# Performance work log

Measured on AMD Instinct MI355X. Metric: run time of the kernel, lower is better.

## Reference

```python
import jax, jax.numpy as jnp
import numpy as np

N_HEADS = 8
D_K = 256
SCALE = D_K ** -0.5


def setup_inputs() -> dict:
    key = jax.random.key(0)
    k1, k2, k3 = jax.random.split(key, 3)
    B, C, H, W = 8, 256, 32, 32
    x = jax.random.normal(k1, (B, C, H, W), dtype=jnp.float32)
    Wp = jax.random.normal(k2, (C, N_HEADS * D_K * 3), dtype=jnp.float32) * (C ** -0.5)
    bp = jnp.zeros((N_HEADS * D_K * 3,), dtype=jnp.float32)
    Wo = jax.random.normal(k3, (N_HEADS * D_K, C), dtype=jnp.float32) * ((N_HEADS * D_K) ** -0.5)
    bo = jnp.zeros((C,), dtype=jnp.float32)
    return {"x": x, "Wp": Wp, "bp": bp, "Wo": Wo, "bo": bo}


def reference(x, Wp, bp, Wo, bo):
    B, C, H, W = x.shape
    S = H * W
    # [B,C,H,W] -> [B,S,C] tokens
    xt = x.reshape(B, C, S).transpose(0, 2, 1)
    qkv = (xt @ Wp + bp).reshape(B, S, N_HEADS, 3 * D_K)
    q, k, v = jnp.split(qkv, 3, axis=-1)  # each [B,S,H,dk]
    attn = jnp.einsum('bihd,bjhd->bijh', q, k) * SCALE
    attn = jax.nn.softmax(attn, axis=2)  # over j (keys)
    res = jnp.einsum('bijh,bjhd->bihd', attn, v).reshape(B, S, N_HEADS * D_K)
    res = res @ Wo + bo + xt  # residual
    return res.transpose(0, 2, 1).reshape(B, C, H, W)
```

## Files before the change

kernel.cpp:

```cpp
#include <hip/hip_runtime.h>

#define NH    8
#define DK    256
#define SS    1024
#define QSCALE 0.09016844136947155f
#define TSH   8192

using frag8  = __attribute__((ext_vector_type(8))) short;
using f32x4  = __attribute__((ext_vector_type(4))) float;
using f32x16 = __attribute__((ext_vector_type(16))) float;

__device__ __forceinline__ unsigned short f2bf(float f) {
    unsigned int u = __float_as_uint(f);
    return (unsigned short)((u + 0x7FFFu + ((u >> 16) & 1u)) >> 16);
}
__device__ __forceinline__ unsigned int pk2bf(float lo, float hi) {
    unsigned int ul = __float_as_uint(lo), uh = __float_as_uint(hi);
    ul += 0x7FFFu + ((ul >> 16) & 1u);
    uh += 0x7FFFu + ((uh >> 16) & 1u);
    return (ul >> 16) | (uh & 0xFFFF0000u);
}

__device__ __forceinline__ void load_lds16(const void* g, void* l) {
    __builtin_amdgcn_global_load_lds(
        (const __attribute__((address_space(1))) unsigned int*)g,
        (__attribute__((address_space(3))) unsigned int*)l, 16, 0, 0);
}


__global__ __launch_bounds__(256) void k0_all(
    const float* __restrict__ x,  unsigned short* __restrict__ xb,
    const float* __restrict__ Wp, unsigned short* __restrict__ Wpt,
    const float* __restrict__ Wo, unsigned short* __restrict__ Wot)
{
    __shared__ float tile[32][33];
    const int bid = blockIdx.x;
    const float* in; unsigned short* out; int R, C, c0, r0;
    if (bid < 2048) {
        int rr = bid;
        in = x + (size_t)(rr >> 8) * 256 * 1024;
        out = xb + (size_t)(rr >> 8) * 256 * 1024;
        R = 256; C = 1024; c0 = (rr & 31) * 32; r0 = ((rr >> 5) & 7) * 32;
    } else if (bid < 3584) {
        int rr = bid - 2048;
        in = Wp; out = Wpt; R = 256; C = 6144;
        c0 = (rr % 192) * 32; r0 = (rr / 192) * 32;
    } else {
        int rr = bid - 3584;
        in = Wo; out = Wot; R = 2048; C = 256;
        c0 = (rr & 7) * 32; r0 = (rr >> 3) * 32;
    }
    const int tx = threadIdx.x & 31, ty = threadIdx.x >> 5;
#pragma unroll
    for (int j = 0; j < 4; j++)
        tile[ty + j * 8][tx] = in[(size_t)(r0 + ty + j * 8) * C + c0 + tx];
    __syncthreads();
#pragma unroll
    for (int j = 0; j < 4; j++)
        out[(size_t)(c0 + ty + j * 8) * R + r0 + tx] = f2bf(tile[tx][ty + j * 8]);
}

__global__ __launch_bounds__(512) void k1_qkv(
    const unsigned short* __restrict__ xb, const unsigned short* __restrict__ Wpt,
    const float* __restrict__ bp,
    unsigned short* __restrict__ qb, unsigned short* __restrict__ kb,
    unsigned short* __restrict__ vb)
{
    __shared__ unsigned short As[2][256 * 32];
    __shared__ unsigned short Bs[2][128 * 32];
    const int t = threadIdx.x;
    const int wave = t >> 6, lane = t & 63;
    const int quad = lane >> 4, l16 = lane & 15;
    const int n0 = blockIdx.x * 128, m0 = blockIdx.y * 256;
    const int b = m0 >> 10, s0 = m0 & 1023;
    const int lr = lane >> 2, lc = (lane & 3) * 8;

    const int h = n0 / 768;
    const int rem = n0 - h * 768;
    const int tt = rem >> 8;

    const int aoff = (tt < 2) ? (wave & 1) * 64 : (wave >> 1) * 64;
    const int boff = (tt < 2) ? (wave >> 1) * 64 : (wave & 1) * 64;

    const unsigned short* Ag = xb + (size_t)(b * 1024 + s0) * 256;
    const unsigned short* Bg = Wpt + (size_t)n0 * 256;

    f32x4 acc[4][4];
#pragma unroll
    for (int i = 0; i < 4; i++)
#pragma unroll
        for (int j = 0; j < 4; j++) acc[i][j] = (f32x4){0.f, 0.f, 0.f, 0.f};

    auto stage = [&](int buf, int kt) {
        const int k0 = kt * 32;
#pragma unroll
        for (int j = 0; j < 2; j++) {
            int ch = wave + j * 8;
            load_lds16(Ag + (size_t)(ch * 16 + lr) * 256 + k0 + lc, &As[buf][ch * 512]);
        }
        load_lds16(Bg + (size_t)(wave * 16 + lr) * 256 + k0 + lc, &Bs[buf][wave * 512]);
    };

    stage(0, 0);
    __syncthreads();

    for (int kt = 0; kt < 8; kt++) {
        const int cur = kt & 1;
        if (kt < 7) stage(cur ^ 1, kt + 1);
        const unsigned short* Fa = (tt < 2) ? &Bs[cur][0] : &As[cur][0];
        const unsigned short* Fb = (tt < 2) ? &As[cur][0] : &Bs[cur][0];
        frag8 af[4], bf[4];
#pragma unroll
        for (int i = 0; i < 4; i++)
            af[i] = *(const frag8*)(&Fa[(aoff + i * 16 + l16) * 32 + quad * 8]);
#pragma unroll
        for (int j = 0; j < 4; j++)
            bf[j] = *(const frag8*)(&Fb[(boff + j * 16 + l16) * 32 + quad * 8]);
#pragma unroll
        for (int i = 0; i < 4; i++)
#pragma unroll
            for (int j = 0; j < 4; j++)
                acc[i][j] = __builtin_amdgcn_mfma_f32_16x16x32_bf16(af[i], bf[j], acc[i][j], 0, 0, 0);
        __syncthreads();
    }

    const int dcol0 = rem & 255;
    const size_t bh = (size_t)(b * NH + h);

    if (tt < 2) {
        const float sc = (tt == 0) ? QSCALE : 1.0f;
        unsigned short* dst = (tt == 0 ? qb : kb) + bh * 32 * TSH;
#pragma unroll
        for (int i = 0; i < 4; i++) {
            const int mloc = aoff + i * 16;
            float4 b4 = *(const float4*)(&bp[n0 + mloc + quad * 4]);
            const int octet = ((dcol0 + mloc) >> 3) + (quad >> 1);
            const int drem4 = (quad & 1) * 4;
#pragma unroll
            for (int j = 0; j < 4; j++) {
                const int s = s0 + boff + j * 16 + l16;
                unsigned short* cell = dst + (size_t)(s >> 5) * TSH
                                     + octet * 256 + (s & 31) * 8 + drem4;
                uint2 st;
                st.x = pk2bf((acc[i][j][0] + b4.x) * sc, (acc[i][j][1] + b4.y) * sc);
                st.y = pk2bf((acc[i][j][2] + b4.z) * sc, (acc[i][j][3] + b4.w) * sc);
                *(uint2*)cell = st;
            }
        }
    } else {
        unsigned short* dst = vb + bh * 32 * TSH;
        const int chunk = (quad & 1) * 2048;
        const int jjb = (quad & 2) * 2;
        float bias[4];
#pragma unroll
        for (int j = 0; j < 4; j++) bias[j] = bp[n0 + boff + j * 16 + l16];
#pragma unroll
        for (int j = 0; j < 4; j++) {
            int d = dcol0 + boff + j * 16 + l16;
#pragma unroll
            for (int i = 0; i < 4; i++) {
                int g = ((aoff >> 4) + i) & 1;
                size_t tile = (size_t)((s0 + aoff + i * 16) >> 5) * TSH;
                uint2 st;
                st.x = pk2bf(acc[i][j][0] + bias[j], acc[i][j][1] + bias[j]);
                st.y = pk2bf(acc[i][j][2] + bias[j], acc[i][j][3] + bias[j]);
                *(uint2*)(&dst[tile + g * 4096 + chunk + d * 8 + jjb]) = st;
            }
        }
    }
}

__global__ __launch_bounds__(256, 2) void k2_attn(
    const unsigned short* __restrict__ qb, const unsigned short* __restrict__ kb,
    const unsigned short* __restrict__ vb, unsigned short* __restrict__ ob)
{
    __shared__ unsigned short Ks[2][TSH];
    __shared__ unsigned short Vs[2][TSH];

    const int t = threadIdx.x;
    const int wave = t >> 6, lane = t & 63;
    const int l32 = lane & 31, hw = lane >> 5;

    const int flat = blockIdx.x;
    const int xcd = flat & 7, tt2 = flat >> 3;
    const int qt = tt2 & 7;
    const int bh = xcd * 8 + (tt2 >> 3);

    const int qrow0 = qt * 128 + wave * 32;

    frag8 qf[16];
    {
        const unsigned short* qp = qb + ((size_t)bh * 32 + qt * 4 + wave) * TSH
                                 + hw * 256 + l32 * 8;
#pragma unroll
        for (int s = 0; s < 16; s++) qf[s] = *(const frag8*)(qp + s * 512);
    }

    f32x16 acc[8];
#pragma unroll
    for (int nb = 0; nb < 8; nb++)
#pragma unroll
        for (int r = 0; r < 16; r++) acc[nb][r] = 0.f;
    float lsum = 0.f;

    const unsigned short* kstg = kb + (size_t)bh * 32 * TSH + wave * 2048 + lane * 8;
    const unsigned short* vstg = vb + (size_t)bh * 32 * TSH + wave * 2048 + lane * 8;

    auto prefetch = [&](int buf, int kt) {
#pragma unroll
        for (int j = 0; j < 4; j++) {
            load_lds16(kstg + (size_t)kt * TSH + j * 512, &Ks[buf][wave * 2048 + j * 512]);
            load_lds16(vstg + (size_t)kt * TSH + j * 512, &Vs[buf][wave * 2048 + j * 512]);
        }
    };

    auto body = [&](const unsigned short* Kb, const unsigned short* Vb) {
        f32x16 sa0, sa1;
#pragma unroll
        for (int r = 0; r < 16; r++) { sa0[r] = 0.f; sa1[r] = 0.f; }
        __builtin_amdgcn_s_setprio(1);
#pragma unroll
        for (int s = 0; s < 16; s += 2) {
            frag8 kf0 = *(const frag8*)(Kb + (2 * s + hw) * 256 + l32 * 8);
            frag8 kf1 = *(const frag8*)(Kb + (2 * s + 2 + hw) * 256 + l32 * 8);
            sa0 = __builtin_amdgcn_mfma_f32_32x32x16_bf16(kf0, qf[s], sa0, 0, 0, 0);
            sa1 = __builtin_amdgcn_mfma_f32_32x32x16_bf16(kf1, qf[s + 1], sa1, 0, 0, 0);
        }
        __builtin_amdgcn_s_setprio(0);
        float p[16];
#pragma unroll
        for (int e = 0; e < 16; e++) {
            p[e] = exp2f(sa0[e] + sa1[e]);
            lsum += p[e];
        }
        frag8 pf[2];
#pragma unroll
        for (int g = 0; g < 2; g++) {
            uint4 w;
            w.x = pk2bf(p[g * 8 + 0], p[g * 8 + 1]);
            w.y = pk2bf(p[g * 8 + 2], p[g * 8 + 3]);
            w.z = pk2bf(p[g * 8 + 4], p[g * 8 + 5]);
            w.w = pk2bf(p[g * 8 + 6], p[g * 8 + 7]);
            pf[g] = *(frag8*)&w;
        }
        __builtin_amdgcn_s_setprio(1);
#pragma unroll
        for (int g = 0; g < 2; g++)
#pragma unroll
            for (int nb = 0; nb < 8; nb++) {
                frag8 vf = *(const frag8*)(Vb + (g * 2 + hw) * 2048 + (nb * 32 + l32) * 8);
                acc[nb] = __builtin_amdgcn_mfma_f32_32x32x16_bf16(pf[g], vf, acc[nb], 0, 0, 0);
            }
        __builtin_amdgcn_s_setprio(0);
    };

    prefetch(0, 0);
    asm volatile("s_waitcnt vmcnt(0)" ::: "memory");
    __builtin_amdgcn_s_barrier();
    for (int kt = 0; kt < 30; kt += 2) {
        prefetch(1, kt + 1);
        asm volatile("s_waitcnt vmcnt(8)" ::: "memory");
        __builtin_amdgcn_s_barrier();
        body(&Ks[0][0], &Vs[0][0]);
        __builtin_amdgcn_s_barrier();
        prefetch(0, kt + 2);
        asm volatile("s_waitcnt vmcnt(8)" ::: "memory");
        __builtin_amdgcn_s_barrier();
        body(&Ks[1][0], &Vs[1][0]);
        __builtin_amdgcn_s_barrier();
    }
    prefetch(1, 31);
    asm volatile("s_waitcnt vmcnt(8)" ::: "memory");
    __builtin_amdgcn_s_barrier();
    body(&Ks[0][0], &Vs[0][0]);
    asm volatile("s_waitcnt vmcnt(0)" ::: "memory");
    __builtin_amdgcn_s_barrier();
    body(&Ks[1][0], &Vs[1][0]);

    lsum += __shfl_xor(lsum, 32);
    const float linv = 1.f / lsum;

    unsigned short* og = ob + ((size_t)bh * SS + qrow0) * DK + l32;
#pragma unroll
    for (int r = 0; r < 16; r++) {
        const int rowl = (r & 3) + 8 * (r >> 2) + 4 * hw;
        const float li = __shfl(linv, rowl, 64);
        unsigned short* orow = og + (size_t)rowl * DK;
#pragma unroll
        for (int nb = 0; nb < 8; nb++)
            orow[nb * 32] = f2bf(acc[nb][r] * li);
    }
}

__global__ __launch_bounds__(256) void k3_proj(
    const unsigned short* __restrict__ ob, const unsigned short* __restrict__ Wot,
    const float* __restrict__ bo, const float* __restrict__ x,
    float* __restrict__ out)
{
    __shared__ unsigned short As[2][2][2048];
    __shared__ unsigned short Bs[2][2][2048];
    const int t = threadIdx.x;
    const int wave = t >> 6, lane = t & 63;
    const int quad = lane >> 4, l16 = lane & 15;
    const int n0 = blockIdx.x * 64, m0 = blockIdx.y * 64;
    const int b = m0 >> 10, s0 = m0 & 1023;
    const int mq = (wave >> 1) * 32, nq = (wave & 1) * 32;
    const int lr = lane >> 2, lc = (lane & 3) * 8;

    const unsigned short* Bg = Wot + (size_t)n0 * 2048;

    f32x4 acc[2][2];
#pragma unroll
    for (int i = 0; i < 2; i++)
#pragma unroll
        for (int j = 0; j < 2; j++) acc[i][j] = (f32x4){0.f, 0.f, 0.f, 0.f};

    auto stage = [&](int buf, int kt) {
        const int k0 = kt * 64;
        const int h = k0 >> 8, d0 = k0 & 255;
        const unsigned short* Ag = ob + (size_t)((b * 8 + h) * 1024 + s0) * 256 + d0;
#pragma unroll
        for (int sl = 0; sl < 2; sl++) {
            load_lds16(Ag + (size_t)(wave * 16 + lr) * 256 + sl * 32 + lc, &As[buf][sl][wave * 512]);
            load_lds16(Bg + (size_t)(wave * 16 + lr) * 2048 + k0 + sl * 32 + lc, &Bs[buf][sl][wave * 512]);
        }
    };

    stage(0, 0);
    __syncthreads();

    for (int kt = 0; kt < 32; kt++) {
        const int cur = kt & 1;
        if (kt < 31) stage(cur ^ 1, kt + 1);
#pragma unroll
        for (int sl = 0; sl < 2; sl++) {
            frag8 af[2], bf[2];
#pragma unroll
            for (int i = 0; i < 2; i++)
                af[i] = *(const frag8*)(&As[cur][sl][(mq + i * 16 + l16) * 32 + quad * 8]);
#pragma unroll
            for (int j = 0; j < 2; j++)
                bf[j] = *(const frag8*)(&Bs[cur][sl][(nq + j * 16 + l16) * 32 + quad * 8]);
#pragma unroll
            for (int i = 0; i < 2; i++)
#pragma unroll
                for (int j = 0; j < 2; j++)
                    acc[i][j] = __builtin_amdgcn_mfma_f32_16x16x32_bf16(af[i], bf[j], acc[i][j], 0, 0, 0);
        }
        __syncthreads();
    }

#pragma unroll
    for (int j = 0; j < 2; j++) {
        int c = n0 + nq + j * 16 + l16;
        float bias = bo[c];
#pragma unroll
        for (int i = 0; i < 2; i++) {
            int s = s0 + mq + i * 16 + quad * 4;
            size_t off = (size_t)(b * 256 + c) * 1024 + s;
            float4 xv = *(const float4*)(&x[off]);
            float4 ov;
            ov.x = acc[i][j][0] + bias + xv.x;
            ov.y = acc[i][j][1] + bias + xv.y;
            ov.z = acc[i][j][2] + bias + xv.z;
            ov.w = acc[i][j][3] + bias + xv.w;
            *(float4*)(&out[off]) = ov;
        }
    }
}

extern "C" void kernel_launch(void* const* d_in, const int* in_sizes, int n_in,
                              void* d_out, int out_size, void* d_ws, size_t ws_size,
                              hipStream_t stream)
{
    const float* x  = (const float*)d_in[0];
    const float* Wp = (const float*)d_in[1];
    const float* bp = (const float*)d_in[2];
    const float* Wo = (const float*)d_in[3];
    const float* bo = (const float*)d_in[4];
    float* out = (float*)d_out;

    char* ws = (char*)d_ws;
    unsigned short* qb  = (unsigned short*)(ws);
    unsigned short* kb  = (unsigned short*)(ws + 33554432);
    unsigned short* vb  = (unsigned short*)(ws + 67108864);
    unsigned short* xb  = (unsigned short*)(ws + 100663296);
    unsigned short* Wpt = (unsigned short*)(ws + 104857600);
    unsigned short* Wot = (unsigned short*)(ws + 108003328);

    k0_all<<<dim3(4096), 256, 0, stream>>>(x, xb, Wp, Wpt, Wo, Wot);
    k1_qkv<<<dim3(48, 32), 512, 0, stream>>>(xb, Wpt, bp, qb, kb, vb);
    k2_attn<<<dim3(512), 256, 0, stream>>>(qb, kb, vb, qb );
    k3_proj<<<dim3(4, 128), 256, 0, stream>>>(qb, Wot, bo, x, out);
}
```

Baseline: 219.2 us.

## Software-pipeline PV matmul of previous tile with QK and softmax of current tile

The attention loop is restructured so that the P·V MFMAs for key tile kt-1 are issued after the QK^T MFMAs of tile kt and before its exp2 and bf16 packing. The aim is to overlap the transcendental and packing ALU work with matrix-core work inside one wave. V staging becomes triple-buffered so tile kt-1's V stays resident while tile kt+1 is prefetched, and the s_setprio hints are dropped. This raises LDS per block from 64KB to 80KB, which may limit two blocks per CU, and keeps the P fragments live across iterations.

```diff
diff --git a/kernel.cpp b/kernel.cpp
--- a/kernel.cpp
+++ b/kernel.cpp
@@ -175,7 +175,7 @@
     const unsigned short* __restrict__ vb, unsigned short* __restrict__ ob)
 {
     __shared__ unsigned short Ks[2][TSH];
-    __shared__ unsigned short Vs[2][TSH];
+    __shared__ unsigned short Vs[3][TSH];
 
     const int t = threadIdx.x;
     const int wave = t >> 6, lane = t & 63;
@@ -206,19 +206,40 @@
     const unsigned short* kstg = kb + (size_t)bh * 32 * TSH + wave * 2048 + lane * 8;
     const unsigned short* vstg = vb + (size_t)bh * 32 * TSH + wave * 2048 + lane * 8;
 
-    auto prefetch = [&](int buf, int kt) {
+    auto prefetch = [&](int kbuf, int vbuf, int kt) {
 #pragma unroll
         for (int j = 0; j < 4; j++) {
-            load_lds16(kstg + (size_t)kt * TSH + j * 512, &Ks[buf][wave * 2048 + j * 512]);
-            load_lds16(vstg + (size_t)kt * TSH + j * 512, &Vs[buf][wave * 2048 + j * 512]);
+            load_lds16(kstg + (size_t)kt * TSH + j * 512, &Ks[kbuf][wave * 2048 + j * 512]);
+            load_lds16(vstg + (size_t)kt * TSH + j * 512, &Vs[vbuf][wave * 2048 + j * 512]);
         }
     };
 
-    auto body = [&](const unsigned short* Kb, const unsigned short* Vb) {
+    frag8 pfr[2];
+
+    auto pv = [&](const unsigned short* Vb) {
+#pragma unroll
+        for (int g = 0; g < 2; g++)
+#pragma unroll
+            for (int nb = 0; nb < 8; nb++) {
+                frag8 vf = *(const frag8*)(Vb + (g * 2 + hw) * 2048 + (nb * 32 + l32) * 8);
+                acc[nb] = __builtin_amdgcn_mfma_f32_32x32x16_bf16(pfr[g], vf, acc[nb], 0, 0, 0);
+            }
+    };
+
+    prefetch(0, 0, 0);
+    for (int kt = 0; kt < 32; kt++) {
+        if (kt < 31) {
+            prefetch((kt + 1) & 1, (kt + 1) % 3, kt + 1);
+            asm volatile("s_waitcnt vmcnt(8)" ::: "memory");
+        } else {
+            asm volatile("s_waitcnt vmcnt(0)" ::: "memory");
+        }
+        __builtin_amdgcn_s_barrier();
+
+        const unsigned short* Kb = &Ks[kt & 1][0];
         f32x16 sa0, sa1;
 #pragma unroll
         for (int r = 0; r < 16; r++) { sa0[r] = 0.f; sa1[r] = 0.f; }
-        __builtin_amdgcn_s_setprio(1);
 #pragma unroll
         for (int s = 0; s < 16; s += 2) {
             frag8 kf0 = *(const frag8*)(Kb + (2 * s + hw) * 256 + l32 * 8);
@@ -226,14 +247,15 @@
             sa0 = __builtin_amdgcn_mfma_f32_32x32x16_bf16(kf0, qf[s], sa0, 0, 0, 0);
             sa1 = __builtin_amdgcn_mfma_f32_32x32x16_bf16(kf1, qf[s + 1], sa1, 0, 0, 0);
         }
-        __builtin_amdgcn_s_setprio(0);
+
+        if (kt > 0) pv(&Vs[(kt + 2) % 3][0]);
+
         float p[16];
 #pragma unroll
         for (int e = 0; e < 16; e++) {
             p[e] = exp2f(sa0[e] + sa1[e]);
             lsum += p[e];
         }
-        frag8 pf[2];
 #pragma unroll
         for (int g = 0; g < 2; g++) {
             uint4 w;
@@ -241,41 +263,12 @@
             w.y = pk2bf(p[g * 8 + 2], p[g * 8 + 3]);
             w.z = pk2bf(p[g * 8 + 4], p[g * 8 + 5]);
             w.w = pk2bf(p[g * 8 + 6], p[g * 8 + 7]);
-            pf[g] = *(frag8*)&w;
-        }
-        __builtin_amdgcn_s_setprio(1);
-#pragma unroll
-        for (int g = 0; g < 2; g++)
-#pragma unroll
-            for (int nb = 0; nb < 8; nb++) {
-                frag8 vf = *(const frag8*)(Vb + (g * 2 + hw) * 2048 + (nb * 32 + l32) * 8);
-                acc[nb] = __builtin_amdgcn_mfma_f32_32x32x16_bf16(pf[g], vf, acc[nb], 0, 0, 0);
-            }
-        __builtin_amdgcn_s_setprio(0);
-    };
-
-    prefetch(0, 0);
-    asm volatile("s_waitcnt vmcnt(0)" ::: "memory");
-    __builtin_amdgcn_s_barrier();
-    for (int kt = 0; kt < 30; kt += 2) {
-        prefetch(1, kt + 1);
-        asm volatile("s_waitcnt vmcnt(8)" ::: "memory");
+            pfr[g] = *(frag8*)&w;
+        }
+
         __builtin_amdgcn_s_barrier();
-        body(&Ks[0][0], &Vs[0][0]);
-        __builtin_amdgcn_s_barrier();
-        prefetch(0, kt + 2);
-        asm volatile("s_waitcnt vmcnt(8)" ::: "memory");
-        __builtin_amdgcn_s_barrier();
-        body(&Ks[1][0], &Vs[1][0]);
-        __builtin_amdgcn_s_barrier();
-    }
-    prefetch(1, 31);
-    asm volatile("s_waitcnt vmcnt(8)" ::: "memory");
-    __builtin_amdgcn_s_barrier();
-    body(&Ks[0][0], &Vs[0][0]);
-    asm volatile("s_waitcnt vmcnt(0)" ::: "memory");
-    __builtin_amdgcn_s_barrier();
-    body(&Ks[1][0], &Vs[1][0]);
+    }
+    pv(&Vs[1][0]);
 
     lsum += __shfl_xor(lsum, 32);
     const float linv = 1.f / lsum;
```

Result: no change. 215.6 us (-1.6%).
